# Performance work log

Hardware: AMD Instinct MI355X
Metric: run time of the kernel (lower is better)

The kernel has to match this reference:

```python
import jax, jax.numpy as jnp
import numpy as np
from jax import lax

DIM = 256; NH = 8; WS = 4; HD = DIM // NH  # head_dim=32
LH = 4; HH = 4; L_DIM = LH * HD; H_DIM = HH * HD  # 128 each
SCALE = HD ** -0.5


def conv2d(x, w, b, padding=0, groups=1):
    y = lax.conv_general_dilated(x, w, (1, 1), [(padding, padding)] * 2,
                                 feature_group_count=groups,
                                 dimension_numbers=('NCHW', 'OIHW', 'NCHW'))
    return y + b[None, :, None, None]


def dsc(x, dww, dwb, pww, pwb):
    # depthwise 3x3 (pad 1) + pointwise 1x1, both with bias
    y = conv2d(x, dww, dwb, padding=1, groups=x.shape[1])
    return conv2d(y, pww, pwb)


def setup_inputs() -> dict:
    key = jax.random.key(0)
    ks = jax.random.split(key, 16)
    p = lambda k, s: jax.random.normal(k, s, jnp.float32) * 0.02
    B, H, W = 8, 96, 96
    return {
        'x': jax.random.normal(ks[0], (B, DIM, H, W), jnp.float32),
        'restore_w': p(ks[1], (DIM, DIM // (WS * WS), 1, 1)), 'restore_b': jnp.zeros((DIM,), jnp.float32),
        'lq_dw_w': p(ks[2], (DIM, 1, 3, 3)), 'lq_dw_b': jnp.zeros((DIM,), jnp.float32),
        'lq_pw_w': p(ks[3], (L_DIM, DIM, 1, 1)), 'lq_pw_b': jnp.zeros((L_DIM,), jnp.float32),
        'lkv_dw_w': p(ks[4], (DIM, 1, 3, 3)), 'lkv_dw_b': jnp.zeros((DIM,), jnp.float32),
        'lkv_pw_w': p(ks[5], (2 * L_DIM, DIM, 1, 1)), 'lkv_pw_b': jnp.zeros((2 * L_DIM,), jnp.float32),
        'lproj_dw_w': p(ks[6], (L_DIM, 1, 3, 3)), 'lproj_dw_b': jnp.zeros((L_DIM,), jnp.float32),
        'lproj_pw_w': p(ks[7], (L_DIM, L_DIM, 1, 1)), 'lproj_pw_b': jnp.zeros((L_DIM,), jnp.float32),
        'hqkv_dw_w': p(ks[8], (DIM, 1, 3, 3)), 'hqkv_dw_b': jnp.zeros((DIM,), jnp.float32),
        'hqkv_pw_w': p(ks[9], (3 * H_DIM, DIM, 1, 1)), 'hqkv_pw_b': jnp.zeros((3 * H_DIM,), jnp.float32),
        'hproj_dw_w': p(ks[10], (H_DIM, 1, 3, 3)), 'hproj_dw_b': jnp.zeros((H_DIM,), jnp.float32),
        'hproj_pw_w': p(ks[11], (H_DIM, H_DIM, 1, 1)), 'hproj_pw_b': jnp.zeros((H_DIM,), jnp.float32),
    }


def reference(x, restore_w, restore_b,
              lq_dw_w, lq_dw_b, lq_pw_w, lq_pw_b,
              lkv_dw_w, lkv_dw_b, lkv_pw_w, lkv_pw_b,
              lproj_dw_w, lproj_dw_b, lproj_pw_w, lproj_pw_b,
              hqkv_dw_w, hqkv_dw_b, hqkv_pw_w, hqkv_pw_b,
              hproj_dw_w, hproj_dw_b, hproj_pw_w, hproj_pw_b):
    B, C, H, W = x.shape
    hg, wg = H // WS, W // WS
    # ---- low/high feature split (avg-pool + PixelShuffle fallback branch) ----
    low = jnp.mean(x.reshape(B, C, hg, WS, wg, WS), axis=(3, 5))  # [B,C,hg,wg]
    c_out = C // (WS * WS)
    lu = low.reshape(B, c_out, WS, WS, hg, wg)
    lu = lu.transpose(0, 1, 4, 2, 5, 3).reshape(B, c_out, H, W)  # PixelShuffle(WS)
    high = conv2d(lu, restore_w, restore_b) - x
    # ---- low-frequency (global) attention: q at full res, kv at pooled res ----
    lq = dsc(x, lq_dw_w, lq_dw_b, lq_pw_w, lq_pw_b)
    lq = lq.reshape(B, LH, HD, H * W).transpose(0, 1, 3, 2)  # [B,LH,HW,HD]
    lkv = dsc(low, lkv_dw_w, lkv_dw_b, lkv_pw_w, lkv_pw_b)
    lkv = lkv.reshape(B, 2, LH, HD, hg * wg).transpose(1, 0, 2, 4, 3)
    lk, lv = lkv[0], lkv[1]  # [B,LH,hg*wg,HD]
    l_attn = jax.nn.softmax(jnp.einsum('bhqd,bhkd->bhqk', lq, lk) * SCALE, axis=-1)
    lx = jnp.einsum('bhqk,bhkd->bhqd', l_attn, lv)  # [B,LH,HW,HD]
    lx = lx.transpose(0, 1, 3, 2).reshape(B, L_DIM, H, W)
    lx = dsc(lx, lproj_dw_w, lproj_dw_b, lproj_pw_w, lproj_pw_b)
    # ---- high-frequency (windowed local) attention ----
    qkv = dsc(high, hqkv_dw_w, hqkv_dw_b, hqkv_pw_w, hqkv_pw_b)
    qkv = qkv.reshape(B, 3 * HH, HD, hg, WS, wg, WS)
    qkv = qkv.transpose(0, 3, 5, 1, 4, 6, 2).reshape(B, hg * wg, 3, HH, WS * WS, HD)
    qkv = qkv.transpose(2, 0, 1, 3, 4, 5)
    hq, hk, hv = qkv[0], qkv[1], qkv[2]  # [B,G,HH,ws2,HD]
    h_attn = jax.nn.softmax(jnp.einsum('bgnqd,bgnkd->bgnqk', hq, hk) * SCALE, axis=-1)
    ho = jnp.einsum('bgnqk,bgnkd->bgnqd', h_attn, hv)  # [B,G,HH,ws2,HD]
    ho = ho.transpose(0, 1, 3, 2, 4).reshape(B, hg, wg, WS, WS, H_DIM)
    ho = ho.transpose(0, 1, 3, 2, 4, 5).reshape(B, H, W, H_DIM).transpose(0, 3, 1, 2)
    hx = dsc(ho, hproj_dw_w, hproj_dw_b, hproj_pw_w, hproj_pw_b)
    return jnp.concatenate([lx, hx], axis=1)  # [B,DIM,H,W]
```

## Files before the change

### kernel.cpp

```cpp
#include <hip/hip_runtime.h>


#define SCALE_F 0.17677669529663687f

typedef unsigned short u16;
typedef __attribute__((ext_vector_type(8))) short bf16x8;
typedef __attribute__((ext_vector_type(4))) float f32x4;
typedef __attribute__((ext_vector_type(8))) u16 u16x8;
typedef __attribute__((ext_vector_type(4))) u16 u16x4;

static __device__ __forceinline__ u16 f2bf(float f) {
    unsigned u = __float_as_uint(f);
    return (u16)((u + 0x7FFF + ((u >> 16) & 1)) >> 16);
}
static __device__ __forceinline__ float bf2f(u16 v) {
    return __uint_as_float((unsigned)v << 16);
}
static __device__ __forceinline__ float ldf(float v) { return v; }
static __device__ __forceinline__ float ldf(u16 v)   { return bf2f(v); }

__global__ __launch_bounds__(256) void pool_kernel(const float* __restrict__ x,
                                                   float* __restrict__ low) {
    int o = blockIdx.x * 256 + threadIdx.x;
    int wg = o % 24;
    int t  = o / 24;
    int hg = t % 24;
    int bc = t / 24;
    const float* xp = x + (size_t)bc * 9216 + (hg * 4) * 96 + wg * 4;
    float s = 0.f;
#pragma unroll
    for (int r = 0; r < 4; r++) {
        float4 v = *(const float4*)(xp + r * 96);
        s += (v.x + v.y) + (v.z + v.w);
    }
    low[o] = s * (1.f / 16.f);
}

__global__ __launch_bounds__(256) void high_kernel(const float* __restrict__ x,
                                                   const float* __restrict__ low,
                                                   const float* __restrict__ rw,
                                                   const float* __restrict__ rb,
                                                   u16* __restrict__ high) {
    int px = blockIdx.x * 256 + threadIdx.x;
    int cg = blockIdx.y;
    int b  = blockIdx.z;
    int h = px / 96, w = px % 96;
    int sub = (h & 3) * 4 + (w & 3);
    const float* lp = low + ((size_t)b * 256 + sub) * 576 + (h >> 2) * 24 + (w >> 2);
    float lv[16];
#pragma unroll
    for (int co = 0; co < 16; co++) lv[co] = lp[(size_t)co * 16 * 576];
    const float* xp = x    + ((size_t)b * 256 + cg * 64) * 9216 + px;
    u16*         hp = high + ((size_t)b * 256 + cg * 64) * 9216 + px;
#pragma unroll 4
    for (int cl = 0; cl < 64; cl++) {
        int c = cg * 64 + cl;
        float a = rb[c] - xp[(size_t)cl * 9216];
#pragma unroll
        for (int co = 0; co < 16; co++)
            a = fmaf(rw[c * 16 + co], lv[co], a);
        hp[(size_t)cl * 9216] = f2bf(a);
    }
}

__global__ __launch_bounds__(256) void wcvt_kernel(const float* __restrict__ s0,
                                                   const float* __restrict__ s1,
                                                   const float* __restrict__ s2,
                                                   const float* __restrict__ s3,
                                                   const float* __restrict__ s4,
                                                   u16* __restrict__ W) {
    int i = blockIdx.x * 256 + threadIdx.x;
    float v;
    if      (i < 32768)  v = s0[i];
    else if (i < 98304)  v = s1[i - 32768];
    else if (i < 114688) v = s2[i - 98304];
    else if (i < 212992) v = s3[i - 114688];
    else                 v = s4[i - 212992];
    W[i] = f2bf(v);
}

template <int C, int IMH, int IMW, typename TIN>
__global__ __launch_bounds__(256) void dw_kernel(const TIN* __restrict__ in,
                                                 const float* __restrict__ dww,
                                                 const float* __restrict__ dwb,
                                                 u16* __restrict__ Y) {
    constexpr int HW = IMH * IMW;
    constexpr int NSTRIP = HW / 8;
    const int strip = blockIdx.x * 32 + (threadIdx.x >> 3);
    if (strip >= NSTRIP) return;
    const int icq = threadIdx.x & 7;
    const int icg = blockIdx.y, b = blockIdx.z;
    const int ic  = icg * 8 + icq;
    const int px0 = strip * 8;
    const int h   = px0 / IMW, w0 = px0 % IMW;

    const TIN* ip = in + ((size_t)b * C + ic) * HW;
    float r[3][8], lh[3], rh[3];
#pragma unroll
    for (int dr = 0; dr < 3; dr++) {
        int hh = h + dr - 1;
        if (hh < 0 || hh >= IMH) {
#pragma unroll
            for (int j = 0; j < 8; j++) r[dr][j] = 0.f;
            lh[dr] = 0.f; rh[dr] = 0.f;
        } else {
            const TIN* rp = ip + hh * IMW + w0;
            if constexpr (sizeof(TIN) == 4) {
                float4 a = *(const float4*)rp;
                float4 c = *(const float4*)(rp + 4);
                r[dr][0] = a.x; r[dr][1] = a.y; r[dr][2] = a.z; r[dr][3] = a.w;
                r[dr][4] = c.x; r[dr][5] = c.y; r[dr][6] = c.z; r[dr][7] = c.w;
            } else {
                u16x8 a = *(const u16x8*)rp;
#pragma unroll
                for (int j = 0; j < 8; j++) r[dr][j] = bf2f(a[j]);
            }
            lh[dr] = (w0 > 0)           ? ldf(rp[-1]) : 0.f;
            rh[dr] = (w0 + 8 < IMW)     ? ldf(rp[8])  : 0.f;
        }
    }
    const float* wp = dww + ic * 9;
    float wv[9];
#pragma unroll
    for (int t = 0; t < 9; t++) wv[t] = wp[t];
    const float b0 = dwb[ic];

    u16* op = Y + (((size_t)b * (C / 8) + icg) * HW + px0) * 8 + icq;
#pragma unroll
    for (int j = 0; j < 8; j++) {
        float y = b0;
#pragma unroll
        for (int dr = 0; dr < 3; dr++) {
            float l = (j == 0) ? lh[dr] : r[dr][j - 1];
            float m = r[dr][j];
            float rr = (j == 7) ? rh[dr] : r[dr][j + 1];
            y = fmaf(wv[dr * 3 + 0], l, y);
            y = fmaf(wv[dr * 3 + 1], m, y);
            y = fmaf(wv[dr * 3 + 2], rr, y);
        }
        op[j * 8] = f2bf(y);
    }
}

template <int IC, int M, typename TOUT, int MODE>
__global__ __launch_bounds__(256) void pw_gemm(const u16* __restrict__ Y,
                                               const u16* __restrict__ Wmat,
                                               const float* __restrict__ bias,
                                               TOUT* __restrict__ out,
                                               int totc, int ocoff,
                                               u16* __restrict__ qkout,
                                               u16* __restrict__ vout) {
    const int tid  = threadIdx.x;
    const int wave = tid >> 6, lane = tid & 63;
    const int col  = lane & 15, oct = lane >> 4;
    const int mw   = (wave & 1) * 64, nw = (wave >> 1) * 64;
    const int px0    = blockIdx.x * 128;
    const int octile = blockIdx.y;
    const int b      = blockIdx.z;

    __shared__ union {
        struct { u16 W[128 * 72]; u16 Y[8 * 128 * 8]; } g;
        u16 stage[4][64 * 72];
    } lds;
    u16* const Wlds = lds.g.W;
    u16* const Ylds = lds.g.Y;

    f32x4 acc[4][4];
    const f32x4 zero = {0.f, 0.f, 0.f, 0.f};
#pragma unroll
    for (int i = 0; i < 4; i++)
#pragma unroll
        for (int j = 0; j < 4; j++) acc[i][j] = zero;

    const u16* Yb = Y + (size_t)b * (IC / 8) * M * 8;

    for (int kc = 0; kc < IC; kc += 64) {
        __syncthreads();
#pragma unroll
        for (int i = 0; i < 4; i++) {
            int c = tid + i * 256;
            int r = c >> 3, seg = c & 7;
            u16x8 v = *(const u16x8*)(Wmat + (size_t)(octile * 128 + r) * IC + kc + seg * 8);
            *(u16x8*)&Wlds[r * 72 + seg * 8] = v;
        }
#pragma unroll
        for (int i = 0; i < 4; i++) {
            int c = tid + i * 256;
            int ig = c >> 7, pl = c & 127;
            int px = px0 + pl; if (px > M - 1) px = M - 1;
            u16x8 v = *(const u16x8*)(Yb + ((size_t)(kc / 8 + ig) * M + px) * 8);
            *(u16x8*)&Ylds[(ig * 128 + pl) * 8] = v;
        }
        __syncthreads();
#pragma unroll
        for (int kcs = 0; kcs < 2; kcs++) {
            bf16x8 Af[4], Bf[4];
#pragma unroll
            for (int mt = 0; mt < 4; mt++)
                Af[mt] = *(const bf16x8*)&Wlds[(mw + mt * 16 + col) * 72 + kcs * 32 + oct * 8];
#pragma unroll
            for (int nt = 0; nt < 4; nt++)
                Bf[nt] = *(const bf16x8*)&Ylds[((kcs * 4 + oct) * 128 + nw + nt * 16 + col) * 8];
#pragma unroll
            for (int mt = 0; mt < 4; mt++)
#pragma unroll
                for (int nt = 0; nt < 4; nt++)
                    acc[mt][nt] = __builtin_amdgcn_mfma_f32_16x16x32_bf16(
                        Af[mt], Bf[nt], acc[mt][nt], 0, 0, 0);
        }
    }
    if constexpr (MODE == 1) {
        __syncthreads();
        u16* const stg = lds.stage[wave];
#pragma unroll
        for (int mt = 0; mt < 4; mt++)
#pragma unroll
            for (int nt = 0; nt < 4; nt++) {
                u16x4 pk;
#pragma unroll
                for (int i = 0; i < 4; i++) {
                    int oc = octile * 128 + mw + mt * 16 + oct * 4 + i;
                    pk[i] = f2bf(acc[mt][nt][i] + bias[oc]);
                }
                *(u16x4*)&stg[(nt * 16 + col) * 72 + mt * 16 + oct * 4] = pk;
            }
        __syncthreads();
        if (octile < 2) {
            const int p4 = lane >> 2, piece = lane & 3;
#pragma unroll
            for (int pp = 0; pp < 4; pp++) {
                int pl = pp * 16 + p4;
                int px = px0 + nw + pl;
                int h = px / 96, w = px - h * 96;
                int g = (h >> 2) * 24 + (w >> 2);
                int q = (h & 3) * 4 + (w & 3);
                size_t base = (((size_t)b * 576 + g) * 16 + q) * 256
                            + (size_t)(octile * 128 + mw);
#pragma unroll
                for (int half = 0; half < 2; half++) {
                    u16x8 v = *(const u16x8*)&stg[pl * 72 + half * 32 + piece * 8];
                    *(u16x8*)&qkout[base + half * 32 + piece * 8] = v;
                }
            }
        } else {
#pragma unroll
            for (int it = 0; it < 16; it++) {
                int pl0 = it * 4;
                int px = px0 + nw + pl0;
                int h = px / 96, w = px - h * 96;
                int g = (h >> 2) * 24 + (w >> 2);
                int qrow = h & 3;
                int vc = mw + lane;
                u16x4 pk;
#pragma unroll
                for (int j = 0; j < 4; j++) pk[j] = stg[(pl0 + j) * 72 + lane];
                *(u16x4*)&vout[(((size_t)b * 576 + g) * 128 + vc) * 16 + qrow * 4] = pk;
            }
        }
        return;
    }
#pragma unroll
    for (int mt = 0; mt < 4; mt++) {
#pragma unroll
        for (int i = 0; i < 4; i++) {
            int ocl = mw + mt * 16 + oct * 4 + i;
            int oc  = octile * 128 + ocl;
            float bv = bias[oc];
            TOUT* op = out + ((size_t)b * totc + ocoff + oc) * M;
#pragma unroll
            for (int nt = 0; nt < 4; nt++) {
                int px = px0 + nw + nt * 16 + col;
                if (px < M) {
                    float v = acc[mt][nt][i] + bv;
                    if constexpr (sizeof(TOUT) == 2) op[px] = (TOUT)f2bf(v);
                    else                             op[px] = v;
                }
            }
        }
    }
}

__global__ __launch_bounds__(256) void low_attn_mfma(const u16* __restrict__ lq,
                                                     const u16* __restrict__ lkv,
                                                     u16* __restrict__ o) {
    const int qtile = blockIdx.x, head = blockIdx.y, b = blockIdx.z;
    const int tid  = threadIdx.x;
    const int wave = tid >> 6, lane = tid & 63;
    const int col  = lane & 15, oct = lane >> 4;

    __shared__ u16 Klds[288][56];
    __shared__ u16 Vlds[32][296];
    __shared__ u16 Plds[4][16][56];

    const size_t qb  = ((size_t)b * 128 + head * 32) * 9216;
    const size_t kb  = ((size_t)b * 256 + head * 32) * 576;
    const size_t vb  = kb + (size_t)128 * 576;
    const int    q0w = qtile * 256 + wave * 64;

    bf16x8 Qf[4];
#pragma unroll
    for (int qt = 0; qt < 4; qt++)
#pragma unroll
        for (int j = 0; j < 8; j++)
            Qf[qt][j] = (short)lq[qb + (size_t)(oct * 8 + j) * 9216 + q0w + qt * 16 + col];

    bf16x8 ones;
#pragma unroll
    for (int j = 0; j < 8; j++) ones[j] = (short)0x3F80;

    f32x4 Oacc[4][2], Lacc[4];
    const f32x4 zero = {0.f, 0.f, 0.f, 0.f};
#pragma unroll
    for (int qt = 0; qt < 4; qt++) {
        Oacc[qt][0] = zero; Oacc[qt][1] = zero; Lacc[qt] = zero;
    }

    for (int half = 0; half < 2; half++) {
        __syncthreads();
        const int k0 = half * 288;
#pragma unroll
        for (int i = 0; i < 9; i++) {
            int idx = tid + i * 256;
            int d  = idx / 72;
            int kq = (idx % 72) * 4;
            u16x4 kv = *(const u16x4*)(lkv + kb + (size_t)d * 576 + k0 + kq);
            Klds[kq + 0][d] = kv.x;
            Klds[kq + 1][d] = kv.y;
            Klds[kq + 2][d] = kv.z;
            Klds[kq + 3][d] = kv.w;
            *(u16x4*)&Vlds[d][kq] = *(const u16x4*)(lkv + vb + (size_t)d * 576 + k0 + kq);
        }
        __syncthreads();

        for (int kc = 0; kc < 288; kc += 32) {
            bf16x8 Kf0 = *(const bf16x8*)&Klds[kc + col][oct * 8];
            bf16x8 Kf1 = *(const bf16x8*)&Klds[kc + 16 + col][oct * 8];
            bf16x8 Vf0 = *(const bf16x8*)&Vlds[col][kc + oct * 8];
            bf16x8 Vf1 = *(const bf16x8*)&Vlds[16 + col][kc + oct * 8];
#pragma unroll
            for (int qt = 0; qt < 4; qt++) {
                f32x4 S0 = __builtin_amdgcn_mfma_f32_16x16x32_bf16(Qf[qt], Kf0, zero, 0, 0, 0);
                f32x4 S1 = __builtin_amdgcn_mfma_f32_16x16x32_bf16(Qf[qt], Kf1, zero, 0, 0, 0);
#pragma unroll
                for (int i = 0; i < 4; i++) {
                    Plds[wave][oct * 4 + i][col]      = f2bf(__expf(S0[i] * SCALE_F));
                    Plds[wave][oct * 4 + i][16 + col] = f2bf(__expf(S1[i] * SCALE_F));
                }
                bf16x8 Pf = *(const bf16x8*)&Plds[wave][col][oct * 8];
                Oacc[qt][0] = __builtin_amdgcn_mfma_f32_16x16x32_bf16(Pf, Vf0, Oacc[qt][0], 0, 0, 0);
                Oacc[qt][1] = __builtin_amdgcn_mfma_f32_16x16x32_bf16(Pf, Vf1, Oacc[qt][1], 0, 0, 0);
                Lacc[qt]    = __builtin_amdgcn_mfma_f32_16x16x32_bf16(Pf, ones, Lacc[qt], 0, 0, 0);
            }
        }
    }

#pragma unroll
    for (int qt = 0; qt < 4; qt++) {
        f32x4 rl;
#pragma unroll
        for (int i = 0; i < 4; i++) rl[i] = 1.f / Lacc[qt][i];
#pragma unroll
        for (int dh = 0; dh < 2; dh++)
#pragma unroll
            for (int i = 0; i < 4; i++)
                o[qb + (size_t)(dh * 16 + col) * 9216 + q0w + qt * 16 + oct * 4 + i] =
                    f2bf(Oacc[qt][dh][i] * rl[i]);
    }
}

__global__ __launch_bounds__(256) void high_attn_mfma(const u16* __restrict__ qk,
                                                      const u16* __restrict__ v,
                                                      u16* __restrict__ ho) {
    const int wave = threadIdx.x >> 6, lane = threadIdx.x & 63;
    const int col = lane & 15, oct = lane >> 4;
    const int gidx = blockIdx.x * 4 + wave;
    const int b = gidx / 576, g = gidx % 576;

    __shared__ u16 Plds[4][16][36];
    for (int i = lane; i < 16 * 20; i += 64) {
        Plds[wave][i / 20][16 + i % 20] = 0;
    }
    const u16* qkw = qk + (size_t)gidx * 16 * 256;
    const u16* vw  = v  + (size_t)gidx * 128 * 16;
    const int px0  = ((g / 24) * 4) * 96 + (g % 24) * 4;
    u16* ob = ho + (size_t)b * 128 * 9216 + px0;
    const int qy = col >> 2, qx = col & 3;

    const f32x4 zero = {0.f, 0.f, 0.f, 0.f};
    bf16x8 ones;
#pragma unroll
    for (int j = 0; j < 8; j++) ones[j] = (short)0x3F80;

#pragma unroll
    for (int hd = 0; hd < 4; hd++) {
        bf16x8 Qf = *(const bf16x8*)(qkw + col * 256 + hd * 32 + oct * 8);
        bf16x8 Kf = *(const bf16x8*)(qkw + col * 256 + 128 + hd * 32 + oct * 8);
        f32x4 S = __builtin_amdgcn_mfma_f32_16x16x32_bf16(Qf, Kf, zero, 0, 0, 0);
#pragma unroll
        for (int i = 0; i < 4; i++)
            Plds[wave][oct * 4 + i][col] = f2bf(__expf(S[i] * SCALE_F));
        bf16x8 Pf = *(const bf16x8*)&Plds[wave][col][oct * 8];
        bf16x8 Vf0 = *(const bf16x8*)(vw + (hd * 32 + col) * 16 + oct * 8);
        bf16x8 Vf1 = *(const bf16x8*)(vw + (hd * 32 + 16 + col) * 16 + oct * 8);
        f32x4 O0 = __builtin_amdgcn_mfma_f32_16x16x32_bf16(Vf0, Pf, zero, 0, 0, 0);
        f32x4 O1 = __builtin_amdgcn_mfma_f32_16x16x32_bf16(Vf1, Pf, zero, 0, 0, 0);
        f32x4 Ld = __builtin_amdgcn_mfma_f32_16x16x32_bf16(ones, Pf, zero, 0, 0, 0);
        float rl = 1.f / Ld[0];
#pragma unroll
        for (int i = 0; i < 4; i++) {
            ob[(size_t)(hd * 32 + oct * 4 + i) * 9216 + qy * 96 + qx]      = f2bf(O0[i] * rl);
            ob[(size_t)(hd * 32 + 16 + oct * 4 + i) * 9216 + qy * 96 + qx] = f2bf(O1[i] * rl);
        }
    }
}

extern "C" void kernel_launch(void* const* d_in, const int* in_sizes, int n_in,
                              void* d_out, int out_size, void* d_ws, size_t ws_size,
                              hipStream_t stream) {
    const float* x         = (const float*)d_in[0];
    const float* restore_w = (const float*)d_in[1];
    const float* restore_b = (const float*)d_in[2];
    const float* lq_dw_w   = (const float*)d_in[3];
    const float* lq_dw_b   = (const float*)d_in[4];
    const float* lq_pw_w   = (const float*)d_in[5];
    const float* lq_pw_b   = (const float*)d_in[6];
    const float* lkv_dw_w  = (const float*)d_in[7];
    const float* lkv_dw_b  = (const float*)d_in[8];
    const float* lkv_pw_w  = (const float*)d_in[9];
    const float* lkv_pw_b  = (const float*)d_in[10];
    const float* lpr_dw_w  = (const float*)d_in[11];
    const float* lpr_dw_b  = (const float*)d_in[12];
    const float* lpr_pw_w  = (const float*)d_in[13];
    const float* lpr_pw_b  = (const float*)d_in[14];
    const float* hq_dw_w   = (const float*)d_in[15];
    const float* hq_dw_b   = (const float*)d_in[16];
    const float* hq_pw_w   = (const float*)d_in[17];
    const float* hq_pw_b   = (const float*)d_in[18];
    const float* hp_dw_w   = (const float*)d_in[19];
    const float* hp_dw_b   = (const float*)d_in[20];
    const float* hp_pw_w   = (const float*)d_in[21];
    const float* hp_pw_b   = (const float*)d_in[22];
    float* out = (float*)d_out;
    char*  wsb = (char*)d_ws;

    u16*   Wbf    = (u16*)  (wsb + 0);
    float* low    = (float*)(wsb + 524288);
    u16*   highbf = (u16*)  (wsb + 5242880);
    u16*   ho     = (u16*)  (wsb + 5242880);
    u16*   Yhproj = (u16*)  (wsb + 24117248);
    u16*   Ylq    = (u16*)  (wsb + 80740352);
    u16*   Yhqkv  = (u16*)  (wsb + 80740352);
    u16*   lqbf   = (u16*)  (wsb + 118489088);
    u16*   QKwin  = (u16*)  (wsb + 118489088);
    u16*   Vwin   = (u16*)  (wsb + 156237824);
    u16*   Ylkv   = (u16*)  (wsb + 137363456);
    u16*   lkvbf  = (u16*)  (wsb + 139722752);
    u16*   attnL  = (u16*)  (wsb + 142082048);
    u16*   Ylproj = (u16*)  (wsb + 160956416);

    const u16* wlq    = Wbf;
    const u16* wlkv   = Wbf + 32768;
    const u16* wlproj = Wbf + 98304;
    const u16* whqkv  = Wbf + 114688;
    const u16* whproj = Wbf + 212992;

    wcvt_kernel<<<896, 256, 0, stream>>>(lq_pw_w, lkv_pw_w, lpr_pw_w, hq_pw_w, hp_pw_w, Wbf);
    pool_kernel<<<4608, 256, 0, stream>>>(x, low);
    high_kernel<<<dim3(36, 4, 8), 256, 0, stream>>>(x, low, restore_w, restore_b, highbf);

    dw_kernel<256, 96, 96, float><<<dim3(36, 32, 8), 256, 0, stream>>>(x, lq_dw_w, lq_dw_b, Ylq);
    pw_gemm<256, 9216, u16, 0><<<dim3(72, 1, 8), 256, 0, stream>>>(
        Ylq, wlq, lq_pw_b, lqbf, 128, 0, nullptr, nullptr);

    dw_kernel<256, 24, 24, float><<<dim3(3, 32, 8), 256, 0, stream>>>(low, lkv_dw_w, lkv_dw_b, Ylkv);
    pw_gemm<256, 576, u16, 0><<<dim3(5, 2, 8), 256, 0, stream>>>(
        Ylkv, wlkv, lkv_pw_b, lkvbf, 256, 0, nullptr, nullptr);

    low_attn_mfma<<<dim3(36, 4, 8), 256, 0, stream>>>(lqbf, lkvbf, attnL);

    dw_kernel<128, 96, 96, u16><<<dim3(36, 16, 8), 256, 0, stream>>>(attnL, lpr_dw_w, lpr_dw_b, Ylproj);
    pw_gemm<128, 9216, float, 0><<<dim3(72, 1, 8), 256, 0, stream>>>(
        Ylproj, wlproj, lpr_pw_b, out, 256, 0, nullptr, nullptr);

    dw_kernel<256, 96, 96, u16><<<dim3(36, 32, 8), 256, 0, stream>>>(highbf, hq_dw_w, hq_dw_b, Yhqkv);
    pw_gemm<256, 9216, u16, 1><<<dim3(72, 3, 8), 256, 0, stream>>>(
        Yhqkv, whqkv, hq_pw_b, QKwin, 384, 0, QKwin, Vwin);

    high_attn_mfma<<<1152, 256, 0, stream>>>(QKwin, Vwin, ho);

    dw_kernel<128, 96, 96, u16><<<dim3(36, 16, 8), 256, 0, stream>>>(ho, hp_dw_w, hp_dw_b, Yhproj);
    pw_gemm<128, 9216, float, 0><<<dim3(72, 1, 8), 256, 0, stream>>>(
        Yhproj, whproj, hp_pw_b, out, 256, 128, nullptr, nullptr);
}
```

Measured before the change: 545.5 us.

## Compute transposed scores in low attention and shuffle P via bpermute instead of LDS

The low-frequency attention kernel now computes S^T = K·Q^T so each lane holds scores for a single query column. The exponentiated probabilities are packed to bf16 with v_cvt_pk_bf16_f32 and moved into MFMA operand layout with ds_bpermute instead of a round trip through shared memory. The row-sum is now accumulated in registers and reduced with two shuffles, replacing the extra MFMA against a ones vector. This removes per-tile LDS writes and reads and one MFMA per tile, at the cost of four bpermutes per tile and a changed output write pattern.

```diff
diff --git a/kernel.cpp b/kernel.cpp
--- a/kernel.cpp
+++ b/kernel.cpp
@@ -290,7 +290,6 @@
 
     __shared__ u16 Klds[288][56];
     __shared__ u16 Vlds[32][296];
-    __shared__ u16 Plds[4][16][56];
 
     const size_t qb  = ((size_t)b * 128 + head * 32) * 9216;
     const size_t kb  = ((size_t)b * 256 + head * 32) * 576;
@@ -304,16 +303,17 @@
         for (int j = 0; j < 8; j++)
             Qf[qt][j] = (short)lq[qb + (size_t)(oct * 8 + j) * 9216 + q0w + qt * 16 + col];
 
-    bf16x8 ones;
-#pragma unroll
-    for (int j = 0; j < 8; j++) ones[j] = (short)0x3F80;
-
-    f32x4 Oacc[4][2], Lacc[4];
+    f32x4 Oacc[4][2];
+    float Lpart[4];
     const f32x4 zero = {0.f, 0.f, 0.f, 0.f};
 #pragma unroll
     for (int qt = 0; qt < 4; qt++) {
-        Oacc[qt][0] = zero; Oacc[qt][1] = zero; Lacc[qt] = zero;
-    }
+        Oacc[qt][0] = zero; Oacc[qt][1] = zero; Lpart[qt] = 0.f;
+    }
+
+    const bool lo32  = (lane < 32);
+    const int  addrA = ((oct & 1) * 32 + col) * 4;
+    const int  addrB = addrA + 64;
 
     for (int half = 0; half < 2; half++) {
         __syncthreads();
@@ -339,32 +339,46 @@
             bf16x8 Vf1 = *(const bf16x8*)&Vlds[16 + col][kc + oct * 8];
 #pragma unroll
             for (int qt = 0; qt < 4; qt++) {
-                f32x4 S0 = __builtin_amdgcn_mfma_f32_16x16x32_bf16(Qf[qt], Kf0, zero, 0, 0, 0);
-                f32x4 S1 = __builtin_amdgcn_mfma_f32_16x16x32_bf16(Qf[qt], Kf1, zero, 0, 0, 0);
+                f32x4 S0 = __builtin_amdgcn_mfma_f32_16x16x32_bf16(Kf0, Qf[qt], zero, 0, 0, 0);
+                f32x4 S1 = __builtin_amdgcn_mfma_f32_16x16x32_bf16(Kf1, Qf[qt], zero, 0, 0, 0);
+                float p0[4], p1[4];
 #pragma unroll
                 for (int i = 0; i < 4; i++) {
-                    Plds[wave][oct * 4 + i][col]      = f2bf(__expf(S0[i] * SCALE_F));
-                    Plds[wave][oct * 4 + i][16 + col] = f2bf(__expf(S1[i] * SCALE_F));
+                    p0[i] = __expf(S0[i] * SCALE_F);
+                    p1[i] = __expf(S1[i] * SCALE_F);
                 }
-                bf16x8 Pf = *(const bf16x8*)&Plds[wave][col][oct * 8];
-                Oacc[qt][0] = __builtin_amdgcn_mfma_f32_16x16x32_bf16(Pf, Vf0, Oacc[qt][0], 0, 0, 0);
-                Oacc[qt][1] = __builtin_amdgcn_mfma_f32_16x16x32_bf16(Pf, Vf1, Oacc[qt][1], 0, 0, 0);
-                Lacc[qt]    = __builtin_amdgcn_mfma_f32_16x16x32_bf16(Pf, ones, Lacc[qt], 0, 0, 0);
+                Lpart[qt] += (p0[0] + p0[1]) + (p0[2] + p0[3])
+                           + (p1[0] + p1[1]) + (p1[2] + p1[3]);
+                unsigned a0, a1, b0, b1;
+                asm("v_cvt_pk_bf16_f32 %0, %1, %2" : "=v"(a0) : "v"(p0[0]), "v"(p0[1]));
+                asm("v_cvt_pk_bf16_f32 %0, %1, %2" : "=v"(a1) : "v"(p0[2]), "v"(p0[3]));
+                asm("v_cvt_pk_bf16_f32 %0, %1, %2" : "=v"(b0) : "v"(p1[0]), "v"(p1[1]));
+                asm("v_cvt_pk_bf16_f32 %0, %1, %2" : "=v"(b1) : "v"(p1[2]), "v"(p1[3]));
+                int s0 = lo32 ? (int)a0 : (int)b0;
+                int s1 = lo32 ? (int)a1 : (int)b1;
+                union { int w[4]; bf16x8 v; } bu;
+                bu.w[0] = __builtin_amdgcn_ds_bpermute(addrA, s0);
+                bu.w[1] = __builtin_amdgcn_ds_bpermute(addrA, s1);
+                bu.w[2] = __builtin_amdgcn_ds_bpermute(addrB, s0);
+                bu.w[3] = __builtin_amdgcn_ds_bpermute(addrB, s1);
+                Oacc[qt][0] = __builtin_amdgcn_mfma_f32_16x16x32_bf16(Vf0, bu.v, Oacc[qt][0], 0, 0, 0);
+                Oacc[qt][1] = __builtin_amdgcn_mfma_f32_16x16x32_bf16(Vf1, bu.v, Oacc[qt][1], 0, 0, 0);
             }
         }
     }
 
 #pragma unroll
     for (int qt = 0; qt < 4; qt++) {
-        f32x4 rl;
-#pragma unroll
-        for (int i = 0; i < 4; i++) rl[i] = 1.f / Lacc[qt][i];
+        float L = Lpart[qt];
+        L += __shfl_xor(L, 16);
+        L += __shfl_xor(L, 32);
+        float rl = 1.f / L;
 #pragma unroll
         for (int dh = 0; dh < 2; dh++)
 #pragma unroll
             for (int i = 0; i < 4; i++)
-                o[qb + (size_t)(dh * 16 + col) * 9216 + q0w + qt * 16 + oct * 4 + i] =
-                    f2bf(Oacc[qt][dh][i] * rl[i]);
+                o[qb + (size_t)(dh * 16 + oct * 4 + i) * 9216 + q0w + qt * 16 + col] =
+                    f2bf(Oacc[qt][dh][i] * rl);
     }
 }
 
```

Result: slower. 585.8 us (+7.4%).
